# Performance work log

Measured on AMD Instinct MI355X. Metric: run time of the kernel, lower is better.

## Reference

```python
import jax, jax.numpy as jnp
from jax import lax
import numpy as np

# Dims
B_, CIN, COUT, T = 2, 64, 128, 8192
K, NM, N, DCONV, EXP = 5, 2, 16, 4, 2   # kernel, n_mamba, d_state, d_conv, expand
DI = EXP * COUT                          # d_inner = 256
DTR = (COUT + 15) // 16                  # dt_rank = 8
M = NM * 2                               # mamba instances (fwd+bwd per block)


def setup_inputs() -> dict:
    key = jax.random.key(0)
    ks = jax.random.split(key, 8)
    r = lambda k, s, sc=0.02: (jax.random.normal(k, s) * sc).astype(jnp.float32)
    return {
        "x": jax.random.normal(ks[0], (B_, CIN, T), dtype=jnp.float32),
        "conv_w": r(ks[1], (COUT, CIN, K), 0.05),
        "conv_b": jnp.zeros((COUT,), jnp.float32),
        "gn_g": jnp.ones((COUT,), jnp.float32),
        "gn_b": jnp.zeros((COUT,), jnp.float32),
        "prelu_a": jnp.full((1,), 0.25, jnp.float32),
        "ln_g": jnp.ones((NM, COUT), jnp.float32),
        "ln_b": jnp.zeros((NM, COUT), jnp.float32),
        "W_in": r(ks[2], (M, 2 * DI, COUT)),
        "conv1d_w": r(ks[3], (M, DI, 1, DCONV), 0.1),
        "conv1d_b": jnp.zeros((M, DI), jnp.float32),
        "W_xproj": r(ks[4], (M, DTR + 2 * N, DI)),
        "W_dt": r(ks[5], (M, DI, DTR), 0.1),
        "b_dt": jnp.full((M, DI), -4.0, jnp.float32),
        "A_log": jnp.broadcast_to(jnp.log(jnp.arange(1, N + 1, dtype=jnp.float32)), (M, DI, N)).copy(),
        "D_param": jnp.ones((M, DI), jnp.float32),
        "W_out": r(ks[6], (M, COUT, DI)),
    }


def _silu(x):
    return x * jax.nn.sigmoid(x)


def _layernorm(x, g, b, eps=1e-5):
    mu = x.mean(-1, keepdims=True)
    v = ((x - mu) ** 2).mean(-1, keepdims=True)
    return (x - mu) * lax.rsqrt(v + eps) * g + b


def _mamba(h, Wi, cw, cb, Wx, Wd, bd, Alog, Dp, Wo):
    # h: [B, L, d_model] -> [B, L, d_model]. Standard Mamba (S6) block.
    Bb, L, _ = h.shape
    xz = jnp.einsum('bld,ed->ble', h, Wi)               # [B,L,2*DI]
    xp, z = jnp.split(xz, 2, axis=-1)
    xc = jnp.transpose(xp, (0, 2, 1))                   # [B,DI,L]
    xc = lax.conv_general_dilated(xc, cw, (1,), [(DCONV - 1, 0)],
                                  feature_group_count=DI,
                                  dimension_numbers=('NCH', 'OIH', 'NCH')) + cb[None, :, None]
    u = _silu(jnp.transpose(xc, (0, 2, 1)))             # [B,L,DI]
    xdbl = jnp.einsum('bld,ed->ble', u, Wx)             # [B,L,DTR+2N]
    dt, Bm, Cm = jnp.split(xdbl, [DTR, DTR + N], axis=-1)
    delta = jax.nn.softplus(jnp.einsum('blr,dr->bld', dt, Wd) + bd)  # [B,L,DI]
    A = -jnp.exp(Alog)                                  # [DI,N]
    dA = jnp.exp(delta[..., None] * A)                  # [B,L,DI,N]
    dBu = (delta * u)[..., None] * Bm[:, :, None, :]    # [B,L,DI,N]

    def step(hc, inp):
        a, b, c = inp
        hc = a * hc + b                                  # [B,DI,N]
        return hc, jnp.einsum('bdn,bn->bd', hc, c)

    h0 = jnp.zeros((Bb, DI, N), dtype=h.dtype)
    _, ys = lax.scan(step, h0, (jnp.moveaxis(dA, 1, 0), jnp.moveaxis(dBu, 1, 0), jnp.moveaxis(Cm, 1, 0)))
    y = jnp.moveaxis(ys, 0, 1) + u * Dp                 # [B,L,DI]
    y = y * _silu(z)
    return jnp.einsum('ble,de->bld', y, Wo)


def reference(x, conv_w, conv_b, gn_g, gn_b, prelu_a, ln_g, ln_b, W_in,
              conv1d_w, conv1d_b, W_xproj, W_dt, b_dt, A_log, D_param, W_out):
    # Conv1d stride 2, padding K//2: [B,CIN,T] -> [B,COUT,T//2]
    h = lax.conv_general_dilated(x, conv_w, (2,), [(K // 2, K // 2)],
                                 dimension_numbers=('NCH', 'OIH', 'NCH')) + conv_b[None, :, None]
    # GroupNorm(1, COUT): normalize jointly over (C, T)
    mu = h.mean((1, 2), keepdims=True)
    v = ((h - mu) ** 2).mean((1, 2), keepdims=True)
    h = (h - mu) * lax.rsqrt(v + 1e-5) * gn_g[None, :, None] + gn_b[None, :, None]
    h = jnp.where(h >= 0, h, prelu_a[0] * h)            # PReLU (shared scalar)
    h = jnp.transpose(h, (0, 2, 1))                     # [B, L, C]
    for i in range(NM):
        hn = _layernorm(h, ln_g[i], ln_b[i])
        f, bw = 2 * i, 2 * i + 1
        yf = _mamba(hn, W_in[f], conv1d_w[f], conv1d_b[f], W_xproj[f], W_dt[f], b_dt[f], A_log[f], D_param[f], W_out[f])
        hb = jnp.flip(hn, axis=1)
        yb = jnp.flip(_mamba(hb, W_in[bw], conv1d_w[bw], conv1d_b[bw], W_xproj[bw], W_dt[bw], b_dt[bw], A_log[bw], D_param[bw], W_out[bw]), axis=1)
        h = h + yf + yb                                  # bidirectional residual
    return jnp.transpose(h, (0, 2, 1))                   # [B, COUT, T//2]
```

## Files before the change

kernel.cpp:

```cpp
#include <hip/hip_runtime.h>
#include <hip/hip_bf16.h>
#include <math.h>

constexpr int B2   = 2;
constexpr int CIN  = 64;
constexpr int COUT = 128;
constexpr int T    = 8192;
constexpr int L    = 4096;
constexpr int DI   = 256;
constexpr int NST  = 16;
constexpr int DTR  = 8;
constexpr int Q    = 32;
constexpr int NC   = 128;
constexpr int TOK  = B2 * L;

typedef __attribute__((ext_vector_type(8))) short bf16x8s;
typedef __attribute__((ext_vector_type(4))) float f32x4;

__device__ __forceinline__ float sigmoidf_(float x) { return 1.f / (1.f + __expf(-x)); }
__device__ __forceinline__ unsigned short f2bf(float f) {
    unsigned int u = __float_as_uint(f);
    unsigned int r = (u + 0x7FFFu + ((u >> 16) & 1u)) >> 16;
    return (unsigned short)r;
}
__device__ __forceinline__ float bf2f(unsigned short s) {
    return __uint_as_float((unsigned int)s << 16);
}

__global__ __launch_bounds__(256) void prep_all_kernel(
    const float* __restrict__ W_in, const float* __restrict__ W_out,
    const float* __restrict__ cw,
    unsigned short* __restrict__ Winb, unsigned short* __restrict__ Woutb,
    unsigned short* __restrict__ Wrb, float* __restrict__ stats) {
    int idx = blockIdx.x * 256 + threadIdx.x;
    if (blockIdx.x == 0 && threadIdx.x < 4) stats[threadIdx.x] = 0.f;
    if (idx < 262144) {
        Winb[idx] = f2bf(W_in[idx]);
    } else if (idx < 393216) {
        int i = idx - 262144; Woutb[i] = f2bf(W_out[i]);
    } else if (idx < 434176) {
        int i = idx - 393216;
        int co = i / 320, r = i % 320;
        int kp = r >> 6, ci = r & 63;
        Wrb[i] = f2bf(cw[co * 320 + ci * 5 + kp]);
    }
}

__global__ __launch_bounds__(256) void xpose_kernel(
    const float* __restrict__ x, unsigned short* __restrict__ xTb) {
    __shared__ float tile[64][65];
    int b = blockIdx.y, tb = blockIdx.x * 64, tid = threadIdx.x;
    #pragma unroll
    for (int i = 0; i < 16; ++i) {
        int idx = i * 256 + tid; int ci = idx >> 6, tt = idx & 63;
        tile[ci][tt] = x[((size_t)b * CIN + ci) * T + tb + tt];
    }
    __syncthreads();
    #pragma unroll
    for (int i = 0; i < 16; ++i) {
        int idx = i * 256 + tid; int tt = idx >> 6, ci = idx & 63;
        xTb[((size_t)b * T + tb + tt) * 64 + ci] = f2bf(tile[ci][tt]);
    }
}

__global__ __launch_bounds__(256) void conv_mfma_kernel(
    const unsigned short* __restrict__ xTb, const unsigned short* __restrict__ Wrb,
    const float* __restrict__ cb, float* __restrict__ h, float* __restrict__ stats) {
    const int tid = threadIdx.x;
    const int w = tid >> 6, lane = tid & 63, q = lane >> 4, c = lane & 15;
    const int t0g = blockIdx.x * 64;
    const int t0  = t0g + w * 16;
    const int ct0 = blockIdx.y * 64;
    const int b   = t0g >> 12;
    const int l   = (t0 + c) & (L - 1);
    f32x4 acc[4] = {};
    for (int kc = 0; kc < 320; kc += 32) {
        int kp  = kc >> 6;
        int ci0 = (kc & 63) + q * 8;
        int p = 2 * l + kp - 2;
        bf16x8s a = {};
        if (p >= 0 && p < T)
            a = *(const bf16x8s*)&xTb[((size_t)b * T + p) * 64 + ci0];
        #pragma unroll
        for (int i = 0; i < 4; ++i) {
            bf16x8s bb = *(const bf16x8s*)&Wrb[(size_t)(ct0 + i * 16 + c) * 320 + kc + q * 8];
            acc[i] = __builtin_amdgcn_mfma_f32_16x16x32_bf16(a, bb, acc[i], 0, 0, 0);
        }
    }
    float s = 0.f, ss = 0.f;
    #pragma unroll
    for (int i = 0; i < 4; ++i) {
        int cout = ct0 + i * 16 + c;
        float bias = cb[cout];
        #pragma unroll
        for (int r = 0; r < 4; ++r) {
            int tok = t0 + q * 4 + r;
            float v = acc[i][r] + bias;
            h[(size_t)tok * COUT + cout] = v;
            s += v; ss += v * v;
        }
    }
    #pragma unroll
    for (int off = 32; off; off >>= 1) {
        s  += __shfl_down(s,  off, 64);
        ss += __shfl_down(ss, off, 64);
    }
    if (lane == 0) {
        atomicAdd(&stats[b * 2 + 0], s);
        atomicAdd(&stats[b * 2 + 1], ss);
    }
}

__global__ __launch_bounds__(256) void gn_ln_kernel(
    float* __restrict__ h, const float* __restrict__ gn_g,
    const float* __restrict__ gn_b, const float* __restrict__ prelu_a,
    const float* __restrict__ stats, unsigned short* __restrict__ hnb,
    const float* __restrict__ lng, const float* __restrict__ lnb) {
    int wave = threadIdx.x >> 6, lane = threadIdx.x & 63;
    int t = blockIdx.x * 4 + wave;
    int b = t >> 12;
    const float n = (float)(L * COUT);
    float mu   = stats[b * 2 + 0] / n;
    float var  = stats[b * 2 + 1] / n - mu * mu;
    float rstd = rsqrtf(var + 1e-5f);
    float a = prelu_a[0];
    float* row = h + (size_t)t * COUT;
    float2 v  = *(const float2*)&row[lane * 2];
    float2 g  = *(const float2*)&gn_g[lane * 2];
    float2 bb = *(const float2*)&gn_b[lane * 2];
    v.x = (v.x - mu) * rstd * g.x + bb.x; v.x = v.x >= 0.f ? v.x : a * v.x;
    v.y = (v.y - mu) * rstd * g.y + bb.y; v.y = v.y >= 0.f ? v.y : a * v.y;
    *(float2*)&row[lane * 2] = v;
    float s = v.x + v.y, ss = v.x * v.x + v.y * v.y;
    #pragma unroll
    for (int off = 32; off; off >>= 1) {
        s  += __shfl_xor(s,  off, 64);
        ss += __shfl_xor(ss, off, 64);
    }
    float mu2 = s * (1.f / 128.f);
    float var2 = ss * (1.f / 128.f) - mu2 * mu2;
    float rstd2 = rsqrtf(var2 + 1e-5f);
    float2 gg = *(const float2*)&lng[lane * 2];
    float2 lb = *(const float2*)&lnb[lane * 2];
    ushort2 o;
    o.x = f2bf((v.x - mu2) * rstd2 * gg.x + lb.x);
    o.y = f2bf((v.y - mu2) * rstd2 * gg.y + lb.y);
    *(ushort2*)&hnb[(size_t)t * COUT + lane * 2] = o;
}

__global__ __launch_bounds__(256) void ln_kernel(
    const float* __restrict__ h, unsigned short* __restrict__ hnb,
    const float* __restrict__ g, const float* __restrict__ bta) {
    int wave = threadIdx.x >> 6, lane = threadIdx.x & 63;
    int t = blockIdx.x * 4 + wave;
    const float* row = h + (size_t)t * COUT;
    float2 v = *(const float2*)&row[lane * 2];
    float s = v.x + v.y, ss = v.x * v.x + v.y * v.y;
    #pragma unroll
    for (int off = 32; off; off >>= 1) {
        s  += __shfl_xor(s,  off, 64);
        ss += __shfl_xor(ss, off, 64);
    }
    float mu = s * (1.f / 128.f);
    float var = ss * (1.f / 128.f) - mu * mu;
    float rstd = rsqrtf(var + 1e-5f);
    float2 gg = *(const float2*)&g[lane * 2];
    float2 bb = *(const float2*)&bta[lane * 2];
    ushort2 o;
    o.x = f2bf((v.x - mu) * rstd * gg.x + bb.x);
    o.y = f2bf((v.y - mu) * rstd * gg.y + bb.y);
    *(ushort2*)&hnb[(size_t)t * COUT + lane * 2] = o;
}

__global__ __launch_bounds__(256) void inproj_dw_kernel(
    const unsigned short* __restrict__ hnb, const unsigned short* __restrict__ Winb,
    const float* __restrict__ cw, const float* __restrict__ cbias,
    float* __restrict__ u0, float* __restrict__ u1,
    unsigned short* __restrict__ zb0, unsigned short* __restrict__ zb1, int layer) {
    __shared__ float xs[80 * 68];
    const int tid = threadIdx.x;
    const int w = tid >> 6, lane = tid & 63, q = lane >> 4, c = lane & 15;
    const int tBase = blockIdx.x * 64;
    const int nBase = blockIdx.y * 64;
    const int inst = nBase >> 9;
    const int e0 = nBase & 511;
    const int m = layer * 2 + inst;
    const unsigned short* Wb = Winb + (size_t)m * 512 * 128;

    if (e0 >= 256) {
        const int t0 = tBase + w * 16;
        f32x4 acc[4] = {};
        for (int kc = 0; kc < 128; kc += 32) {
            bf16x8s a = *(const bf16x8s*)&hnb[(size_t)(t0 + c) * 128 + kc + q * 8];
            #pragma unroll
            for (int i = 0; i < 4; ++i) {
                bf16x8s bb = *(const bf16x8s*)&Wb[(size_t)(e0 + i * 16 + c) * 128 + kc + q * 8];
                acc[i] = __builtin_amdgcn_mfma_f32_16x16x32_bf16(a, bb, acc[i], 0, 0, 0);
            }
        }
        unsigned short* zb = inst ? zb1 : zb0;
        #pragma unroll
        for (int i = 0; i < 4; ++i) {
            int eo = (e0 + i * 16 + c) & 255;
            #pragma unroll
            for (int r = 0; r < 4; ++r) {
                int tok = t0 + q * 4 + r;
                float v = acc[i][r];
                zb[(size_t)tok * DI + eo] = f2bf(v * sigmoidf_(v));
            }
        }
        return;
    }
    const int winT0 = (inst == 0) ? (tBase - 16) : tBase;
    for (int pass = 0; pass < 2; ++pass) {
        if (pass == 1 && w != 0) break;
        int slot = (pass == 0) ? (w + (inst == 0 ? 1 : 0))
                               : ((inst == 0) ? 0 : 4);
        int tokA = winT0 + slot * 16 + c;
        tokA = tokA < 0 ? 0 : (tokA > TOK - 1 ? TOK - 1 : tokA);
        f32x4 acc[4] = {};
        for (int kc = 0; kc < 128; kc += 32) {
            bf16x8s a = *(const bf16x8s*)&hnb[(size_t)tokA * 128 + kc + q * 8];
            #pragma unroll
            for (int i = 0; i < 4; ++i) {
                bf16x8s bb = *(const bf16x8s*)&Wb[(size_t)(e0 + i * 16 + c) * 128 + kc + q * 8];
                acc[i] = __builtin_amdgcn_mfma_f32_16x16x32_bf16(a, bb, acc[i], 0, 0, 0);
            }
        }
        #pragma unroll
        for (int i = 0; i < 4; ++i)
            #pragma unroll
            for (int r = 0; r < 4; ++r)
                xs[(slot * 16 + q * 4 + r) * 68 + i * 16 + c] = acc[i][r];
    }
    __syncthreads();
    const int l0base = tBase & (L - 1);
    const int ch4 = tid & 15;
    const int d0 = e0 + ch4 * 4;
    float4 w0 = *(const float4*)&cw[(size_t)(m * DI + d0 + 0) * 4];
    float4 w1 = *(const float4*)&cw[(size_t)(m * DI + d0 + 1) * 4];
    float4 w2 = *(const float4*)&cw[(size_t)(m * DI + d0 + 2) * 4];
    float4 w3 = *(const float4*)&cw[(size_t)(m * DI + d0 + 3) * 4];
    float4 bias4 = *(const float4*)&cbias[m * DI + d0];
    float* ud = inst ? u1 : u0;
    #pragma unroll
    for (int p = 0; p < 4; ++p) {
        int j = p * 16 + (tid >> 4);
        float4 acc = bias4;
        #pragma unroll
        for (int k = 0; k < 4; ++k) {
            bool valid = (inst == 0) ? (l0base + j - 3 + k >= 0)
                                     : (l0base + j + 3 - k < L);
            if (valid) {
                int wj = (inst == 0) ? (j + 13 + k) : (j + 3 - k);
                float4 v = *(const float4*)&xs[wj * 68 + ch4 * 4];
                float wk0 = ((const float*)&w0)[k], wk1 = ((const float*)&w1)[k];
                float wk2 = ((const float*)&w2)[k], wk3 = ((const float*)&w3)[k];
                acc.x = fmaf(wk0, v.x, acc.x); acc.y = fmaf(wk1, v.y, acc.y);
                acc.z = fmaf(wk2, v.z, acc.z); acc.w = fmaf(wk3, v.w, acc.w);
            }
        }
        acc.x *= sigmoidf_(acc.x); acc.y *= sigmoidf_(acc.y);
        acc.z *= sigmoidf_(acc.z); acc.w *= sigmoidf_(acc.w);
        *(float4*)&ud[(size_t)(tBase + j) * DI + d0] = acc;
    }
}

__global__ __launch_bounds__(256) void xproj_kernel(
    const float* __restrict__ u0, const float* __restrict__ u1,
    const float* __restrict__ Wx,
    float* __restrict__ xd0, float* __restrict__ xd1,
    float* __restrict__ Bm0, float* __restrict__ Bm1,
    float* __restrict__ Cm0, float* __restrict__ Cm1, int layer) {
    __shared__ float red[4][64][21];
    const int tid   = threadIdx.x;
    const int kq    = tid >> 6;
    const int lane  = tid & 63;
    const int eq    = lane & 7;
    const int tq    = lane >> 3;
    const int tBase = blockIdx.x * 32;
    const int inst  = blockIdx.y;
    const int m     = layer * 2 + inst;
    const float* u  = inst ? u1 : u0;
    const float* Wm = Wx + (size_t)m * 40 * 256;
    const int k0 = kq * 64;
    const float* uB = u + (size_t)(tBase + tq * 4) * 256 + k0;
    float acc[5][4] = {};
    #pragma unroll 2
    for (int kk = 0; kk < 64; kk += 4) {
        float4 a[4], w[5];
        #pragma unroll
        for (int j = 0; j < 4; ++j)
            a[j] = *(const float4*)&uB[(size_t)j * 256 + kk];
        #pragma unroll
        for (int i = 0; i < 5; ++i)
            w[i] = *(const float4*)&Wm[(size_t)(eq + i * 8) * 256 + k0 + kk];
        #pragma unroll
        for (int i = 0; i < 5; ++i)
            #pragma unroll
            for (int j = 0; j < 4; ++j) {
                acc[i][j] = fmaf(a[j].x, w[i].x, acc[i][j]);
                acc[i][j] = fmaf(a[j].y, w[i].y, acc[i][j]);
                acc[i][j] = fmaf(a[j].z, w[i].z, acc[i][j]);
                acc[i][j] = fmaf(a[j].w, w[i].w, acc[i][j]);
            }
    }
    #pragma unroll
    for (int i = 0; i < 5; ++i)
        #pragma unroll
        for (int j = 0; j < 4; ++j)
            red[kq][lane][i * 4 + j] = acc[i][j];
    __syncthreads();
    if (kq != 0) return;
    #pragma unroll
    for (int i = 0; i < 5; ++i)
        #pragma unroll
        for (int j = 0; j < 4; ++j)
            acc[i][j] = red[0][lane][i * 4 + j] + red[1][lane][i * 4 + j]
                      + red[2][lane][i * 4 + j] + red[3][lane][i * 4 + j];
    float* xd = inst ? xd1 : xd0;
    float* Bm = inst ? Bm1 : Bm0;
    float* Cm = inst ? Cm1 : Cm0;
    #pragma unroll
    for (int j = 0; j < 4; ++j) {
        int tok = tBase + tq * 4 + j;
        xd[(size_t)tok * DTR + eq]       = acc[0][j];
        Bm[(size_t)tok * NST + eq]       = acc[1][j];
        Bm[(size_t)tok * NST + 8 + eq]   = acc[2][j];
        Cm[(size_t)tok * NST + eq]       = acc[3][j];
        Cm[(size_t)tok * NST + 8 + eq]   = acc[4][j];
    }
}

__device__ __forceinline__ void compute_dls(
    const float* __restrict__ xd, const float* __restrict__ Wdt,
    const float* __restrict__ bdt, int m, int dtile, int b, int l0, int stp,
    float* dls, float* xdL, float* WdtL, float* bdtL) {
    const int tid = threadIdx.x;
    {
        int j = tid >> 3, r = tid & 7;
        xdL[j * 9 + r] = xd[(size_t)(b * L + l0 + stp * j) * DTR + r];
        size_t wbase = ((size_t)m * DI + dtile * 64) * DTR;
        WdtL[tid]       = Wdt[wbase + tid];
        WdtL[tid + 256] = Wdt[wbase + tid + 256];
        if (tid < 64) bdtL[tid] = bdt[m * DI + dtile * 64 + tid];
    }
    __syncthreads();
    {
        int tt = tid & 31, dgrp = tid >> 5;
        float xr[8];
        #pragma unroll
        for (int r = 0; r < 8; ++r) xr[r] = xdL[tt * 9 + r];
        #pragma unroll
        for (int i = 0; i < 8; ++i) {
            int dd = dgrp * 8 + i;
            float a2 = bdtL[dd];
            #pragma unroll
            for (int r = 0; r < 8; ++r) a2 = fmaf(xr[r], WdtL[dd * 8 + r], a2);
            float sp = fmaxf(a2, 0.f) + __logf(1.f + __expf(-fabsf(a2)));
            dls[tt * 69 + dd] = sp;
        }
    }
    __syncthreads();
}

__global__ __launch_bounds__(256) void scan1_kernel(
    const float* __restrict__ xd0, const float* __restrict__ xd1,
    const float* __restrict__ u0,  const float* __restrict__ u1,
    const float* __restrict__ Bm0, const float* __restrict__ Bm1,
    const float* __restrict__ Wdt, const float* __restrict__ bdt,
    const float* __restrict__ A_log,
    float* __restrict__ hend, float* __restrict__ dsumb, int layer) {
    __shared__ float dls[32 * 69];
    __shared__ float xdL[32 * 9];
    __shared__ float WdtL[512];
    __shared__ float bdtL[64];
    const int tid = threadIdx.x;
    const int nq = tid & 3, dlane = tid >> 2;
    const int chunk = blockIdx.x & (NC - 1), dtile = blockIdx.x >> 7;
    const int b = blockIdx.y, inst = blockIdx.z;
    const int m = layer * 2 + inst, dir = inst;
    const int d = dtile * 64 + dlane;
    const float* xd = inst ? xd1 : xd0;
    const float* u  = inst ? u1  : u0;
    const float* Bm = inst ? Bm1 : Bm0;
    const int s0 = chunk * Q;
    const int l0 = dir ? (L - 1 - s0) : s0;
    const int stp = dir ? -1 : 1;
    compute_dls(xd, Wdt, bdt, m, dtile, b, l0, stp, dls, xdL, WdtL, bdtL);
    float4 av = *(const float4*)&A_log[((size_t)m * DI + d) * NST + nq * 4];
    const float a0 = -expf(av.x), a1 = -expf(av.y), a2 = -expf(av.z), a3 = -expf(av.w);
    long iDU = ((long)(b * L + l0)) * DI + d;
    int  iB  = ((b * L + l0) << 4) + nq * 4;
    const long sDU = (long)stp * DI;
    const int  sB  = stp * NST;
    float h0 = 0.f, h1 = 0.f, h2 = 0.f, h3 = 0.f, dsum = 0.f;
    #pragma unroll 4
    for (int t = 0; t < Q; ++t) {
        float dlt = dls[t * 69 + dlane], uu = u[iDU];
        float4 bm = *(const float4*)&Bm[iB];
        float du = dlt * uu;
        h0 = fmaf(__expf(dlt * a0), h0, du * bm.x);
        h1 = fmaf(__expf(dlt * a1), h1, du * bm.y);
        h2 = fmaf(__expf(dlt * a2), h2, du * bm.z);
        h3 = fmaf(__expf(dlt * a3), h3, du * bm.w);
        dsum += dlt;
        iDU += sDU; iB += sB;
    }
    size_t oh = (((size_t)(inst * 2 + b) * DI + d) * NC + chunk) * NST + nq * 4;
    *(float4*)&hend[oh] = make_float4(h0, h1, h2, h3);
    if (nq == 0) dsumb[((size_t)(inst * 2 + b) * NC + chunk) * DI + d] = dsum;
}

__global__ __launch_bounds__(256) void combine_kernel(
    float* __restrict__ hend, const float* __restrict__ dsumb,
    const float* __restrict__ A_log, int layer) {
    int flat = blockIdx.x * 256 + threadIdx.x;
    int n = flat & 15;
    int d = (flat >> 4) & 255;
    int b = (flat >> 12) & 1;
    int inst = flat >> 13;
    int m = layer * 2 + inst;
    float a = -expf(A_log[((size_t)m * DI + d) * NST + n]);
    size_t baseE = (((size_t)(inst * 2 + b) * DI + d) * NC) * NST + n;
    size_t baseD = ((size_t)(inst * 2 + b) * NC) * DI + d;
    float hc = 0.f;
    #pragma unroll 4
    for (int c = 0; c < NC; ++c) {
        float tmp = hend[baseE + (size_t)c * NST];
        hend[baseE + (size_t)c * NST] = hc;
        float ds = dsumb[baseD + (size_t)c * DI];
        hc = fmaf(__expf(a * ds), hc, tmp);
    }
}

__global__ __launch_bounds__(256) void scan2_kernel(
    const float* __restrict__ xd0, const float* __restrict__ xd1,
    const float* __restrict__ u0,  const float* __restrict__ u1,
    const float* __restrict__ Bm0, const float* __restrict__ Bm1,
    const float* __restrict__ Cm0, const float* __restrict__ Cm1,
    unsigned short* __restrict__ zb0, unsigned short* __restrict__ zb1,
    const float* __restrict__ hin, const float* __restrict__ Wdt,
    const float* __restrict__ bdt, const float* __restrict__ A_log,
    const float* __restrict__ Dp, int layer) {
    __shared__ float dls[32 * 69];
    __shared__ float xdL[32 * 9];
    __shared__ float WdtL[512];
    __shared__ float bdtL[64];
    const int tid = threadIdx.x;
    const int nq = tid & 3, dlane = tid >> 2;
    const int chunk = blockIdx.x & (NC - 1), dtile = blockIdx.x >> 7;
    const int b = blockIdx.y, inst = blockIdx.z;
    const int m = layer * 2 + inst, dir = inst;
    const int d = dtile * 64 + dlane;
    const float* xd = inst ? xd1 : xd0;
    const float* u  = inst ? u1  : u0;
    const float* Bm = inst ? Bm1 : Bm0;
    const float* Cm = inst ? Cm1 : Cm0;
    unsigned short* zs = inst ? zb1 : zb0;
    const int s0 = chunk * Q;
    const int l0 = dir ? (L - 1 - s0) : s0;
    const int stp = dir ? -1 : 1;
    compute_dls(xd, Wdt, bdt, m, dtile, b, l0, stp, dls, xdL, WdtL, bdtL);
    float4 av = *(const float4*)&A_log[((size_t)m * DI + d) * NST + nq * 4];
    const float a0 = -expf(av.x), a1 = -expf(av.y), a2 = -expf(av.z), a3 = -expf(av.w);
    const float dpar = Dp[m * DI + d];
    long iDU = ((long)(b * L + l0)) * DI + d;
    int  iB  = ((b * L + l0) << 4) + nq * 4;
    const long sDU = (long)stp * DI;
    const int  sB  = stp * NST;
    float4 hv = *(const float4*)&hin[(((size_t)(inst * 2 + b) * DI + d) * NC + chunk) * NST + nq * 4];
    float h0 = hv.x, h1 = hv.y, h2 = hv.z, h3 = hv.w;
    #pragma unroll 4
    for (int t = 0; t < Q; ++t) {
        float dlt = dls[t * 69 + dlane], uu = u[iDU];
        float4 bm = *(const float4*)&Bm[iB];
        float4 cm = *(const float4*)&Cm[iB];
        float du = dlt * uu;
        h0 = fmaf(__expf(dlt * a0), h0, du * bm.x);
        h1 = fmaf(__expf(dlt * a1), h1, du * bm.y);
        h2 = fmaf(__expf(dlt * a2), h2, du * bm.z);
        h3 = fmaf(__expf(dlt * a3), h3, du * bm.w);
        float yp = h0 * cm.x + h1 * cm.y + h2 * cm.z + h3 * cm.w;
        yp += __shfl_xor(yp, 1, 4);
        yp += __shfl_xor(yp, 2, 4);
        if (nq == 0) {
            float zv = bf2f(zs[iDU]);
            zs[iDU] = f2bf(fmaf(uu, dpar, yp) * zv);
        }
        iDU += sDU; iB += sB;
    }
}

__global__ __launch_bounds__(256) void outproj_mfma_kernel(
    const unsigned short* __restrict__ ygb0, const unsigned short* __restrict__ ygb1,
    const unsigned short* __restrict__ Woutb, float* __restrict__ h,
    float* __restrict__ out, int layer) {
    const int tid = threadIdx.x;
    const int w = tid >> 6, lane = tid & 63, q = lane >> 4, c = lane & 15;
    const int t0 = blockIdx.x * 64 + w * 16;
    const int ct0 = blockIdx.y * 32;
    f32x4 acc[2] = {};
    #pragma unroll
    for (int inst = 0; inst < 2; ++inst) {
        const unsigned short* yg = inst ? ygb1 : ygb0;
        const unsigned short* Wb = Woutb + (size_t)(layer * 2 + inst) * COUT * DI;
        for (int kc = 0; kc < 256; kc += 32) {
            bf16x8s a = *(const bf16x8s*)&yg[(size_t)(t0 + c) * DI + kc + q * 8];
            #pragma unroll
            for (int i = 0; i < 2; ++i) {
                bf16x8s bb = *(const bf16x8s*)&Wb[(size_t)(ct0 + i * 16 + c) * DI + kc + q * 8];
                acc[i] = __builtin_amdgcn_mfma_f32_16x16x32_bf16(a, bb, acc[i], 0, 0, 0);
            }
        }
    }
    if (layer == 0) {
        #pragma unroll
        for (int i = 0; i < 2; ++i) {
            int cout = ct0 + i * 16 + c;
            #pragma unroll
            for (int r = 0; r < 4; ++r) {
                int tok = t0 + q * 4 + r;
                h[(size_t)tok * COUT + cout] += acc[i][r];
            }
        }
    } else {
        int tok0 = t0 + q * 4;
        int b = tok0 >> 12, l = tok0 & (L - 1);
        #pragma unroll
        for (int i = 0; i < 2; ++i) {
            int cout = ct0 + i * 16 + c;
            float4 o;
            o.x = h[(size_t)(tok0 + 0) * COUT + cout] + acc[i][0];
            o.y = h[(size_t)(tok0 + 1) * COUT + cout] + acc[i][1];
            o.z = h[(size_t)(tok0 + 2) * COUT + cout] + acc[i][2];
            o.w = h[(size_t)(tok0 + 3) * COUT + cout] + acc[i][3];
            *(float4*)&out[((size_t)(b * COUT + cout)) * L + l] = o;
        }
    }
}

extern "C" void kernel_launch(void* const* d_in, const int* in_sizes, int n_in,
                              void* d_out, int out_size, void* d_ws, size_t ws_size,
                              hipStream_t stream) {
    const float* x        = (const float*)d_in[0];
    const float* conv_w   = (const float*)d_in[1];
    const float* conv_b   = (const float*)d_in[2];
    const float* gn_g     = (const float*)d_in[3];
    const float* gn_b     = (const float*)d_in[4];
    const float* prelu_a  = (const float*)d_in[5];
    const float* ln_g     = (const float*)d_in[6];
    const float* ln_b     = (const float*)d_in[7];
    const float* W_in     = (const float*)d_in[8];
    const float* conv1d_w = (const float*)d_in[9];
    const float* conv1d_b = (const float*)d_in[10];
    const float* W_xproj  = (const float*)d_in[11];
    const float* W_dt     = (const float*)d_in[12];
    const float* b_dt     = (const float*)d_in[13];
    const float* A_log    = (const float*)d_in[14];
    const float* D_param  = (const float*)d_in[15];
    const float* W_out    = (const float*)d_in[16];

    float* ws = (float*)d_ws;
    float* h     = ws;
    unsigned short* zb0 = (unsigned short*)(ws + 5242880);
    unsigned short* zb1 = (unsigned short*)(ws + 6291456);
    float* u0    = ws + 7340032;
    float* u1    = ws + 9437184;
    float* xd0   = ws + 11534336;
    float* xd1   = ws + 11599872;
    float* Bm0   = ws + 15728640;
    float* Bm1   = ws + 15859712;
    float* Cm0   = ws + 15990784;
    float* Cm1   = ws + 16121856;
    float* hend  = ws + 16252928;
    float* dsumb = ws + 18350080;
    unsigned short* Winb  = (unsigned short*)(ws + 18481152);
    unsigned short* Wrb   = (unsigned short*)(ws + 18612224);
    unsigned short* Woutb = (unsigned short*)(ws + 18632704);
    float* stats = ws + 18698240;
    unsigned short* hnb = (unsigned short*)hend;
    unsigned short* xTb = zb0;
    float* out = (float*)d_out;

    prep_all_kernel<<<1696, 256, 0, stream>>>(W_in, W_out, conv_w, Winb, Woutb, Wrb, stats);
    xpose_kernel<<<dim3(T / 64, B2), 256, 0, stream>>>(x, xTb);
    conv_mfma_kernel<<<dim3(TOK / 64, COUT / 64), 256, 0, stream>>>(xTb, Wrb, conv_b, h, stats);
    gn_ln_kernel<<<TOK / 4, 256, 0, stream>>>(h, gn_g, gn_b, prelu_a, stats, hnb, ln_g, ln_b);

    for (int layer = 0; layer < 2; ++layer) {
        if (layer == 1)
            ln_kernel<<<TOK / 4, 256, 0, stream>>>(h, hnb, ln_g + COUT, ln_b + COUT);
        inproj_dw_kernel<<<dim3(TOK / 64, 16), 256, 0, stream>>>(hnb, Winb, conv1d_w, conv1d_b,
                                                                 u0, u1, zb0, zb1, layer);
        xproj_kernel<<<dim3(TOK / 32, 2), 256, 0, stream>>>(u0, u1, W_xproj,
                                                            xd0, xd1, Bm0, Bm1, Cm0, Cm1, layer);
        scan1_kernel<<<dim3(NC * 4, B2, 2), 256, 0, stream>>>(xd0, xd1, u0, u1, Bm0, Bm1,
                                                              W_dt, b_dt, A_log, hend, dsumb, layer);
        combine_kernel<<<64, 256, 0, stream>>>(hend, dsumb, A_log, layer);
        scan2_kernel<<<dim3(NC * 4, B2, 2), 256, 0, stream>>>(xd0, xd1, u0, u1, Bm0, Bm1, Cm0, Cm1,
                                                              zb0, zb1, hend, W_dt, b_dt,
                                                              A_log, D_param, layer);
        outproj_mfma_kernel<<<dim3(TOK / 64, 4), 256, 0, stream>>>(zb0, zb1, Woutb, h, out, layer);
    }
}
```

Baseline: 395.9 us.

## Compute softplus delta once in xproj and store for both scans

The dt projection and softplus were computed twice per layer, once in each scan kernel's prologue. That prologue staged data in shared memory behind two barriers. Now xproj_kernel keeps the dt-rank projection in shared memory, computes delta for all 256 channels per token and writes it to a new full-size global buffer. Both scans then read delta directly alongside u. This removes the duplicated compute, shared-memory staging and barriers, at the cost of writing and twice reading an extra [tokens, DI] float tensor per instance.

```diff
diff --git a/kernel.cpp b/kernel.cpp
--- a/kernel.cpp
+++ b/kernel.cpp
@@ -268,11 +268,13 @@
 
 __global__ __launch_bounds__(256) void xproj_kernel(
     const float* __restrict__ u0, const float* __restrict__ u1,
-    const float* __restrict__ Wx,
-    float* __restrict__ xd0, float* __restrict__ xd1,
+    const float* __restrict__ Wx, const float* __restrict__ Wdt,
+    const float* __restrict__ bdt,
+    float* __restrict__ dl0, float* __restrict__ dl1,
     float* __restrict__ Bm0, float* __restrict__ Bm1,
     float* __restrict__ Cm0, float* __restrict__ Cm1, int layer) {
     __shared__ float red[4][64][21];
+    __shared__ float xdl[32 * 9];
     const int tid   = threadIdx.x;
     const int kq    = tid >> 6;
     const int lane  = tid & 63;
@@ -311,85 +313,64 @@
         for (int j = 0; j < 4; ++j)
             red[kq][lane][i * 4 + j] = acc[i][j];
     __syncthreads();
-    if (kq != 0) return;
-    #pragma unroll
-    for (int i = 0; i < 5; ++i)
-        #pragma unroll
-        for (int j = 0; j < 4; ++j)
-            acc[i][j] = red[0][lane][i * 4 + j] + red[1][lane][i * 4 + j]
-                      + red[2][lane][i * 4 + j] + red[3][lane][i * 4 + j];
-    float* xd = inst ? xd1 : xd0;
-    float* Bm = inst ? Bm1 : Bm0;
-    float* Cm = inst ? Cm1 : Cm0;
-    #pragma unroll
-    for (int j = 0; j < 4; ++j) {
-        int tok = tBase + tq * 4 + j;
-        xd[(size_t)tok * DTR + eq]       = acc[0][j];
-        Bm[(size_t)tok * NST + eq]       = acc[1][j];
-        Bm[(size_t)tok * NST + 8 + eq]   = acc[2][j];
-        Cm[(size_t)tok * NST + eq]       = acc[3][j];
-        Cm[(size_t)tok * NST + 8 + eq]   = acc[4][j];
-    }
-}
-
-__device__ __forceinline__ void compute_dls(
-    const float* __restrict__ xd, const float* __restrict__ Wdt,
-    const float* __restrict__ bdt, int m, int dtile, int b, int l0, int stp,
-    float* dls, float* xdL, float* WdtL, float* bdtL) {
-    const int tid = threadIdx.x;
-    {
-        int j = tid >> 3, r = tid & 7;
-        xdL[j * 9 + r] = xd[(size_t)(b * L + l0 + stp * j) * DTR + r];
-        size_t wbase = ((size_t)m * DI + dtile * 64) * DTR;
-        WdtL[tid]       = Wdt[wbase + tid];
-        WdtL[tid + 256] = Wdt[wbase + tid + 256];
-        if (tid < 64) bdtL[tid] = bdt[m * DI + dtile * 64 + tid];
+    if (kq == 0) {
+        #pragma unroll
+        for (int i = 0; i < 5; ++i)
+            #pragma unroll
+            for (int j = 0; j < 4; ++j)
+                acc[i][j] = red[0][lane][i * 4 + j] + red[1][lane][i * 4 + j]
+                          + red[2][lane][i * 4 + j] + red[3][lane][i * 4 + j];
+        float* Bm = inst ? Bm1 : Bm0;
+        float* Cm = inst ? Cm1 : Cm0;
+        #pragma unroll
+        for (int j = 0; j < 4; ++j) {
+            int tok = tBase + tq * 4 + j;
+            xdl[(tq * 4 + j) * 9 + eq]       = acc[0][j];
+            Bm[(size_t)tok * NST + eq]       = acc[1][j];
+            Bm[(size_t)tok * NST + 8 + eq]   = acc[2][j];
+            Cm[(size_t)tok * NST + eq]       = acc[3][j];
+            Cm[(size_t)tok * NST + 8 + eq]   = acc[4][j];
+        }
     }
     __syncthreads();
     {
-        int tt = tid & 31, dgrp = tid >> 5;
-        float xr[8];
-        #pragma unroll
-        for (int r = 0; r < 8; ++r) xr[r] = xdL[tt * 9 + r];
-        #pragma unroll
-        for (int i = 0; i < 8; ++i) {
-            int dd = dgrp * 8 + i;
-            float a2 = bdtL[dd];
-            #pragma unroll
-            for (int r = 0; r < 8; ++r) a2 = fmaf(xr[r], WdtL[dd * 8 + r], a2);
+        int d = tid;
+        float wr[8];
+        #pragma unroll
+        for (int r = 0; r < 8; ++r) wr[r] = Wdt[((size_t)m * DI + d) * DTR + r];
+        float bb = bdt[m * DI + d];
+        float* dl = inst ? dl1 : dl0;
+        #pragma unroll 4
+        for (int tt = 0; tt < 32; ++tt) {
+            float a2 = bb;
+            #pragma unroll
+            for (int r = 0; r < 8; ++r) a2 = fmaf(xdl[tt * 9 + r], wr[r], a2);
             float sp = fmaxf(a2, 0.f) + __logf(1.f + __expf(-fabsf(a2)));
-            dls[tt * 69 + dd] = sp;
-        }
-    }
-    __syncthreads();
+            dl[(size_t)(tBase + tt) * DI + d] = sp;
+        }
+    }
 }
 
 __global__ __launch_bounds__(256) void scan1_kernel(
-    const float* __restrict__ xd0, const float* __restrict__ xd1,
+    const float* __restrict__ dl0, const float* __restrict__ dl1,
     const float* __restrict__ u0,  const float* __restrict__ u1,
     const float* __restrict__ Bm0, const float* __restrict__ Bm1,
-    const float* __restrict__ Wdt, const float* __restrict__ bdt,
     const float* __restrict__ A_log,
     float* __restrict__ hend, float* __restrict__ dsumb, int layer) {
-    __shared__ float dls[32 * 69];
-    __shared__ float xdL[32 * 9];
-    __shared__ float WdtL[512];
-    __shared__ float bdtL[64];
     const int tid = threadIdx.x;
     const int nq = tid & 3, dlane = tid >> 2;
     const int chunk = blockIdx.x & (NC - 1), dtile = blockIdx.x >> 7;
     const int b = blockIdx.y, inst = blockIdx.z;
     const int m = layer * 2 + inst, dir = inst;
     const int d = dtile * 64 + dlane;
-    const float* xd = inst ? xd1 : xd0;
+    const float* dl = inst ? dl1 : dl0;
     const float* u  = inst ? u1  : u0;
     const float* Bm = inst ? Bm1 : Bm0;
+    float4 av = *(const float4*)&A_log[((size_t)m * DI + d) * NST + nq * 4];
+    const float a0 = -expf(av.x), a1 = -expf(av.y), a2 = -expf(av.z), a3 = -expf(av.w);
     const int s0 = chunk * Q;
     const int l0 = dir ? (L - 1 - s0) : s0;
     const int stp = dir ? -1 : 1;
-    compute_dls(xd, Wdt, bdt, m, dtile, b, l0, stp, dls, xdL, WdtL, bdtL);
-    float4 av = *(const float4*)&A_log[((size_t)m * DI + d) * NST + nq * 4];
-    const float a0 = -expf(av.x), a1 = -expf(av.y), a2 = -expf(av.z), a3 = -expf(av.w);
     long iDU = ((long)(b * L + l0)) * DI + d;
     int  iB  = ((b * L + l0) << 4) + nq * 4;
     const long sDU = (long)stp * DI;
@@ -397,7 +378,7 @@
     float h0 = 0.f, h1 = 0.f, h2 = 0.f, h3 = 0.f, dsum = 0.f;
     #pragma unroll 4
     for (int t = 0; t < Q; ++t) {
-        float dlt = dls[t * 69 + dlane], uu = u[iDU];
+        float dlt = dl[iDU], uu = u[iDU];
         float4 bm = *(const float4*)&Bm[iB];
         float du = dlt * uu;
         h0 = fmaf(__expf(dlt * a0), h0, du * bm.x);
@@ -435,36 +416,30 @@
 }
 
 __global__ __launch_bounds__(256) void scan2_kernel(
-    const float* __restrict__ xd0, const float* __restrict__ xd1,
+    const float* __restrict__ dl0, const float* __restrict__ dl1,
     const float* __restrict__ u0,  const float* __restrict__ u1,
     const float* __restrict__ Bm0, const float* __restrict__ Bm1,
     const float* __restrict__ Cm0, const float* __restrict__ Cm1,
     unsigned short* __restrict__ zb0, unsigned short* __restrict__ zb1,
-    const float* __restrict__ hin, const float* __restrict__ Wdt,
-    const float* __restrict__ bdt, const float* __restrict__ A_log,
+    const float* __restrict__ hin, const float* __restrict__ A_log,
     const float* __restrict__ Dp, int layer) {
-    __shared__ float dls[32 * 69];
-    __shared__ float xdL[32 * 9];
-    __shared__ float WdtL[512];
-    __shared__ float bdtL[64];
     const int tid = threadIdx.x;
     const int nq = tid & 3, dlane = tid >> 2;
     const int chunk = blockIdx.x & (NC - 1), dtile = blockIdx.x >> 7;
     const int b = blockIdx.y, inst = blockIdx.z;
     const int m = layer * 2 + inst, dir = inst;
     const int d = dtile * 64 + dlane;
-    const float* xd = inst ? xd1 : xd0;
+    const float* dl = inst ? dl1 : dl0;
     const float* u  = inst ? u1  : u0;
     const float* Bm = inst ? Bm1 : Bm0;
     const float* Cm = inst ? Cm1 : Cm0;
     unsigned short* zs = inst ? zb1 : zb0;
+    float4 av = *(const float4*)&A_log[((size_t)m * DI + d) * NST + nq * 4];
+    const float a0 = -expf(av.x), a1 = -expf(av.y), a2 = -expf(av.z), a3 = -expf(av.w);
+    const float dpar = Dp[m * DI + d];
     const int s0 = chunk * Q;
     const int l0 = dir ? (L - 1 - s0) : s0;
     const int stp = dir ? -1 : 1;
-    compute_dls(xd, Wdt, bdt, m, dtile, b, l0, stp, dls, xdL, WdtL, bdtL);
-    float4 av = *(const float4*)&A_log[((size_t)m * DI + d) * NST + nq * 4];
-    const float a0 = -expf(av.x), a1 = -expf(av.y), a2 = -expf(av.z), a3 = -expf(av.w);
-    const float dpar = Dp[m * DI + d];
     long iDU = ((long)(b * L + l0)) * DI + d;
     int  iB  = ((b * L + l0) << 4) + nq * 4;
     const long sDU = (long)stp * DI;
@@ -473,7 +448,7 @@
     float h0 = hv.x, h1 = hv.y, h2 = hv.z, h3 = hv.w;
     #pragma unroll 4
     for (int t = 0; t < Q; ++t) {
-        float dlt = dls[t * 69 + dlane], uu = u[iDU];
+        float dlt = dl[iDU], uu = u[iDU];
         float4 bm = *(const float4*)&Bm[iB];
         float4 cm = *(const float4*)&Cm[iB];
         float du = dlt * uu;
@@ -567,8 +542,8 @@
     unsigned short* zb1 = (unsigned short*)(ws + 6291456);
     float* u0    = ws + 7340032;
     float* u1    = ws + 9437184;
-    float* xd0   = ws + 11534336;
-    float* xd1   = ws + 11599872;
+    float* dl0   = ws + 11534336;
+    float* dl1   = ws + 13631488;
     float* Bm0   = ws + 15728640;
     float* Bm1   = ws + 15859712;
     float* Cm0   = ws + 15990784;
@@ -593,14 +568,13 @@
             ln_kernel<<<TOK / 4, 256, 0, stream>>>(h, hnb, ln_g + COUT, ln_b + COUT);
         inproj_dw_kernel<<<dim3(TOK / 64, 16), 256, 0, stream>>>(hnb, Winb, conv1d_w, conv1d_b,
                                                                  u0, u1, zb0, zb1, layer);
-        xproj_kernel<<<dim3(TOK / 32, 2), 256, 0, stream>>>(u0, u1, W_xproj,
-                                                            xd0, xd1, Bm0, Bm1, Cm0, Cm1, layer);
-        scan1_kernel<<<dim3(NC * 4, B2, 2), 256, 0, stream>>>(xd0, xd1, u0, u1, Bm0, Bm1,
-                                                              W_dt, b_dt, A_log, hend, dsumb, layer);
+        xproj_kernel<<<dim3(TOK / 32, 2), 256, 0, stream>>>(u0, u1, W_xproj, W_dt, b_dt,
+                                                            dl0, dl1, Bm0, Bm1, Cm0, Cm1, layer);
+        scan1_kernel<<<dim3(NC * 4, B2, 2), 256, 0, stream>>>(dl0, dl1, u0, u1, Bm0, Bm1,
+                                                              A_log, hend, dsumb, layer);
         combine_kernel<<<64, 256, 0, stream>>>(hend, dsumb, A_log, layer);
-        scan2_kernel<<<dim3(NC * 4, B2, 2), 256, 0, stream>>>(xd0, xd1, u0, u1, Bm0, Bm1, Cm0, Cm1,
-                                                              zb0, zb1, hend, W_dt, b_dt,
-                                                              A_log, D_param, layer);
+        scan2_kernel<<<dim3(NC * 4, B2, 2), 256, 0, stream>>>(dl0, dl1, u0, u1, Bm0, Bm1, Cm0, Cm1,
+                                                              zb0, zb1, hend, A_log, D_param, layer);
         outproj_mfma_kernel<<<dim3(TOK / 64, 4), 256, 0, stream>>>(zb0, zb1, Woutb, h, out, layer);
     }
 }
```

New measurement: 399.4 us. About the same (+0.9%).
